# Kernel optimization log

Measured on AMD Instinct MI355X. Metric: run time of the kernel, lower is better.

The kernel has to match this reference:

```python
import jax, jax.numpy as jnp
import numpy as np

B, CIN, COUT, H, W, KK = 1, 32, 64, 181, 360, 4
NNZ_PER, NNZ_PER1 = 9, 4


def _make_psi(rng, K, H, W, nnz_per):
    # Sparse DISCO basis in COO form for longitude 0 (shift-invariant in lon).
    E = K * H * nnz_per
    seg = np.repeat(np.arange(K * H, dtype=np.int32), nnz_per)  # k*H + ho
    ho = seg % H
    dlat = rng.integers(-1, 2, size=E).astype(np.int32)
    hi = np.clip(ho + dlat, 0, H - 1).astype(np.int32)
    wi = (rng.integers(-1, 2, size=E).astype(np.int32)) % W
    vals = (rng.normal(size=E) * 0.2).astype(np.float32)
    return seg, hi, wi, vals


def setup_inputs() -> dict:
    rng = np.random.default_rng(0)
    key = jax.random.key(0)
    ks = jax.random.split(key, 5)
    x = jax.random.normal(ks[0], (B, CIN, H, W), dtype=jnp.float32)
    # spherical quadrature weights: sin(colatitude) * cell area
    theta = np.linspace(0.0, np.pi, H)
    qw = (np.sin(theta) * (np.pi / (H - 1)) * (2.0 * np.pi / W)).astype(np.float32)
    qw = np.maximum(qw, 1e-8).reshape(H, 1)
    seg, hi, wi, vals = _make_psi(rng, KK, H, W, NNZ_PER)
    seg1, hi1, wi1, vals1 = _make_psi(rng, 1, H, W, NNZ_PER1)
    w_depth = jax.random.normal(ks[1], (CIN, KK), dtype=jnp.float32) / np.sqrt(KK)
    w_point = jax.random.normal(ks[2], (COUT, CIN), dtype=jnp.float32) / np.sqrt(CIN)
    bias = jax.random.normal(ks[3], (COUT,), dtype=jnp.float32) * 0.02
    return {
        "x": x,
        "quad_w": jnp.asarray(qw),
        "vals": jnp.asarray(vals),
        "seg": jnp.asarray(seg),
        "hi": jnp.asarray(hi),
        "wi": jnp.asarray(wi),
        "w_depth": w_depth,
        "vals1": jnp.asarray(vals1),
        "seg1": jnp.asarray(seg1),
        "hi1": jnp.asarray(hi1),
        "wi1": jnp.asarray(wi1),
        "w_point": w_point,
        "bias": bias,
        "K": KK,
    }


def _disco_contract(x, vals, seg, hi, wi, K):
    # x: [B,C,H,W]; COO psi at lon 0; out[b,c,k,ho,wo] =
    #   sum_{e: seg[e]==k*H+ho} vals[e] * x[b,c,hi[e],(wi[e]+wo) mod W]
    Bq, C, Hq, Wq = x.shape
    rows = x[:, :, hi, :]                                        # [B,C,E,W]
    col = (wi[:, None] + jnp.arange(Wq, dtype=wi.dtype)[None, :]) % Wq  # [E,W]
    rolled = jnp.take_along_axis(rows, col[None, None, :, :], axis=3)   # [B,C,E,W]
    weighted = rolled * vals[None, None, :, None]
    out = jax.ops.segment_sum(weighted.transpose(2, 0, 1, 3), seg,
                              num_segments=K * Hq)               # [K*H,B,C,W]
    return out.reshape(K, Hq, Bq, C, Wq).transpose(2, 3, 0, 1, 4)  # [B,C,K,H,W]


def reference(x, quad_w, vals, seg, hi, wi, w_depth, vals1, seg1, hi1, wi1,
              w_point, bias, K):
    # depthwise DISCO conv (groups=C_in, no bias)
    xq = x * quad_w                                   # quadrature weighting
    xd = _disco_contract(xq, vals, seg, hi, wi, K)    # [B,C,K,H,W]
    y = jnp.einsum("ck,bckhw->bchw", w_depth, xd)     # per-channel K mix
    # pointwise DISCO conv (kernel_shape=1) = CLinear
    yq = y * quad_w
    z = _disco_contract(yq, vals1, seg1, hi1, wi1, 1)[:, :, 0]  # [B,C,H,W]
    out = jnp.einsum("oc,bchw->bohw", w_point, z) + bias[None, :, None, None]
    return out
```

## Files before the change

kernel.cpp:

```cpp
#include <hip/hip_runtime.h>


#define H_    181
#define W_    360
#define CIN_  32
#define COUT_ 64
#define K_    4
#define NNZ_  9
#define NNZ1_ 4
#define HW_   (H_*W_)
#define NT_   (NNZ1_*K_*NNZ_)

__global__ __launch_bounds__(256) void sepconv_one(
    const float* __restrict__ x, const float* __restrict__ quad_w,
    const float* __restrict__ vals, const int* __restrict__ hi,
    const int* __restrict__ wi, const float* __restrict__ w_depth,
    const float* __restrict__ vals1, const int* __restrict__ hi1,
    const int* __restrict__ wi1, const float* __restrict__ w_point,
    const float* __restrict__ bias, float* __restrict__ out)
{
    const int bx = blockIdx.x;
    const int h  = (bx & 7) * 23 + (bx >> 3);
    if (h >= H_) return;
    const int seg = blockIdx.y;
    const int w0  = seg * 64;
    const int pxn = (seg == 5) ? 40 : 64;
    const int gn  = pxn >> 2;
    const int tid = threadIdx.x;

    __shared__ float Tval[NT_];
    __shared__ int   Tbin[NT_];
    __shared__ float S[K_][25];
    __shared__ float C[CIN_][25];
    __shared__ float zs[64][33];

    if (tid < NT_) {
        const int a   = tid / 36;
        const int rem = tid - a * 36;
        const int k   = rem / 9;
        const int j   = rem - k * 9;
        const int e1  = h * NNZ1_ + a;
        const int m   = hi1[e1];
        const int w1  = wi1[e1];
        const int d1  = (w1 == 1) ? 1 : ((w1 == 0) ? 0 : -1);
        const int e   = (k * H_ + m) * NNZ_ + j;
        const int r   = hi[e];
        const int ww  = wi[e];
        const int d   = (ww == 1) ? 1 : ((ww == 0) ? 0 : -1);
        Tval[tid] = vals1[e1] * quad_w[m] * vals[e] * quad_w[r];
        Tbin[tid] = (r - h + 2) * 5 + (d1 + d + 2);
    }
    __syncthreads();

    if (tid < K_ * 25) {
        const int k   = tid / 25;
        const int bin = tid - k * 25;
        float s = 0.f;
        #pragma unroll
        for (int a = 0; a < NNZ1_; ++a)
            #pragma unroll
            for (int j = 0; j < NNZ_; ++j) {
                const int t2 = a * 36 + k * 9 + j;
                if (Tbin[t2] == bin) s += Tval[t2];
            }
        S[k][bin] = s;
    }
    __syncthreads();

    for (int i = tid; i < CIN_ * 25; i += 256) {
        const int c = i / 25, bin = i - c * 25;
        float acc = 0.f;
        #pragma unroll
        for (int k = 0; k < K_; ++k) acc += w_depth[c * K_ + k] * S[k][bin];
        C[c][bin] = acc;
    }
    __syncthreads();

    int rowoff[5];
    #pragma unroll
    for (int rb = 0; rb < 5; ++rb) {
        int r = h - 2 + rb;
        r = (r < 0) ? 0 : ((r > H_ - 1) ? H_ - 1 : r);
        rowoff[rb] = r * W_;
    }

    for (int q = tid; q < CIN_ * 16; q += 256) {
        const int c = q >> 4;
        const int g = q & 15;
        if (g < gn) {
            const int bw = w0 + g * 4;
            const int cA = (bw + W_ - 4) % W_;
            const int cB = bw;
            const int cC = (bw + 4) % W_;
            const float* xc = x + c * HW_;
            const float* Cc = &C[c][0];

            float a0 = 0.f, a1 = 0.f, a2 = 0.f, a3 = 0.f;
            #pragma unroll
            for (int rb = 0; rb < 5; ++rb) {
                const float* xr = xc + rowoff[rb];
                const float4 vA = *(const float4*)(xr + cA);
                const float4 vB = *(const float4*)(xr + cB);
                const float4 vC = *(const float4*)(xr + cC);
                const float k0 = Cc[rb * 5 + 0], k1 = Cc[rb * 5 + 1],
                            k2 = Cc[rb * 5 + 2], k3 = Cc[rb * 5 + 3],
                            k4 = Cc[rb * 5 + 4];
                a0 += k0 * vA.z + k1 * vA.w + k2 * vB.x + k3 * vB.y + k4 * vB.z;
                a1 += k0 * vA.w + k1 * vB.x + k2 * vB.y + k3 * vB.z + k4 * vB.w;
                a2 += k0 * vB.x + k1 * vB.y + k2 * vB.z + k3 * vB.w + k4 * vC.x;
                a3 += k0 * vB.y + k1 * vB.z + k2 * vB.w + k3 * vC.x + k4 * vC.y;
            }
            const int p = g * 4;
            zs[p + 0][c] = a0;
            zs[p + 1][c] = a1;
            zs[p + 2][c] = a2;
            zs[p + 3][c] = a3;
        }
    }
    __syncthreads();

    const int j  = tid & 63;
    const int oh = tid >> 6;
    if (j < pxn) {
        float zr[CIN_];
        #pragma unroll
        for (int c = 0; c < CIN_; ++c) zr[c] = zs[j][c];

        const float* wp = w_point + oh * 16 * CIN_;
        float* op = out + oh * 16 * HW_ + h * W_ + w0 + j;
        #pragma unroll 4
        for (int oo = 0; oo < 16; ++oo) {
            float acc = bias[oh * 16 + oo];
            #pragma unroll
            for (int c = 0; c < CIN_; ++c) acc += wp[oo * CIN_ + c] * zr[c];
            op[oo * HW_] = acc;
        }
    }
}

extern "C" void kernel_launch(void* const* d_in, const int* in_sizes, int n_in,
                              void* d_out, int out_size, void* d_ws, size_t ws_size,
                              hipStream_t stream) {
    const float* x       = (const float*)d_in[0];
    const float* quad_w  = (const float*)d_in[1];
    const float* vals    = (const float*)d_in[2];
    const int*   hi      = (const int*)d_in[4];
    const int*   wi      = (const int*)d_in[5];
    const float* w_depth = (const float*)d_in[6];
    const float* vals1   = (const float*)d_in[7];
    const int*   hi1     = (const int*)d_in[9];
    const int*   wi1     = (const int*)d_in[10];
    const float* w_point = (const float*)d_in[11];
    const float* bias    = (const float*)d_in[12];

    sepconv_one<<<dim3(184, 6), 256, 0, stream>>>(
        x, quad_w, vals, hi, wi, w_depth, vals1, hi1, wi1,
        w_point, bias, (float*)d_out);
}
```

Baseline: 118.8 us.

## Process two longitude segments per block, prefetching the second during the first GEMV

Each block now handles two 64-wide longitude segments instead of one, halving the grid. The per-row stencil-coefficient setup (Tval/S/C tables) is amortized over two segments, and the global loads for the second segment's stencil are issued before the first segment's pointwise GEMV so their latency overlaps that compute. The cost is higher register pressure from two 15-float4 prefetch buffers, which may reduce occupancy, and fewer blocks for the GPU to spread across CUs.

```diff
diff --git a/kernel.cpp b/kernel.cpp
--- a/kernel.cpp
+++ b/kernel.cpp
@@ -22,17 +22,14 @@
     const int bx = blockIdx.x;
     const int h  = (bx & 7) * 23 + (bx >> 3);
     if (h >= H_) return;
-    const int seg = blockIdx.y;
-    const int w0  = seg * 64;
-    const int pxn = (seg == 5) ? 40 : 64;
-    const int gn  = pxn >> 2;
+    const int sp  = blockIdx.y;
     const int tid = threadIdx.x;
 
     __shared__ float Tval[NT_];
     __shared__ int   Tbin[NT_];
     __shared__ float S[K_][25];
     __shared__ float C[CIN_][25];
-    __shared__ float zs[64][33];
+    __shared__ float zs[2][64][33];
 
     if (tid < NT_) {
         const int a   = tid / 36;
@@ -84,58 +81,107 @@
         rowoff[rb] = r * W_;
     }
 
-    for (int q = tid; q < CIN_ * 16; q += 256) {
-        const int c = q >> 4;
-        const int g = q & 15;
-        if (g < gn) {
-            const int bw = w0 + g * 4;
-            const int cA = (bw + W_ - 4) % W_;
-            const int cB = bw;
-            const int cC = (bw + 4) % W_;
-            const float* xc = x + c * HW_;
-            const float* Cc = &C[c][0];
-
-            float a0 = 0.f, a1 = 0.f, a2 = 0.f, a3 = 0.f;
-            #pragma unroll
-            for (int rb = 0; rb < 5; ++rb) {
-                const float* xr = xc + rowoff[rb];
-                const float4 vA = *(const float4*)(xr + cA);
-                const float4 vB = *(const float4*)(xr + cB);
-                const float4 vC = *(const float4*)(xr + cC);
-                const float k0 = Cc[rb * 5 + 0], k1 = Cc[rb * 5 + 1],
-                            k2 = Cc[rb * 5 + 2], k3 = Cc[rb * 5 + 3],
-                            k4 = Cc[rb * 5 + 4];
-                a0 += k0 * vA.z + k1 * vA.w + k2 * vB.x + k3 * vB.y + k4 * vB.z;
-                a1 += k0 * vA.w + k1 * vB.x + k2 * vB.y + k3 * vB.z + k4 * vB.w;
-                a2 += k0 * vB.x + k1 * vB.y + k2 * vB.z + k3 * vB.w + k4 * vC.x;
-                a3 += k0 * vB.y + k1 * vB.z + k2 * vB.w + k3 * vC.x + k4 * vC.y;
-            }
-            const int p = g * 4;
-            zs[p + 0][c] = a0;
-            zs[p + 1][c] = a1;
-            zs[p + 2][c] = a2;
-            zs[p + 3][c] = a3;
-        }
-    }
-    __syncthreads();
-
+    const int g  = tid & 15;
+    const int c0 = tid >> 4;
+    const int c1 = c0 + 16;
     const int j  = tid & 63;
     const int oh = tid >> 6;
-    if (j < pxn) {
-        float zr[CIN_];
-        #pragma unroll
-        for (int c = 0; c < CIN_; ++c) zr[c] = zs[j][c];
-
-        const float* wp = w_point + oh * 16 * CIN_;
-        float* op = out + oh * 16 * HW_ + h * W_ + w0 + j;
-        #pragma unroll 4
-        for (int oo = 0; oo < 16; ++oo) {
-            float acc = bias[oh * 16 + oo];
+
+    const int seg0 = sp * 2 + 0;
+    const int seg1 = sp * 2 + 1;
+    const int gn1  = (seg1 == 5) ? 10 : 16;
+
+    auto load_item = [&](int c, int bw, float4* Lv) {
+        const int cA = (bw + W_ - 4) % W_;
+        const int cB = bw;
+        const int cC = (bw + 4) % W_;
+        const float* xc = x + c * HW_;
+        #pragma unroll
+        for (int rb = 0; rb < 5; ++rb) {
+            const float* xr = xc + rowoff[rb];
+            Lv[rb * 3 + 0] = *(const float4*)(xr + cA);
+            Lv[rb * 3 + 1] = *(const float4*)(xr + cB);
+            Lv[rb * 3 + 2] = *(const float4*)(xr + cC);
+        }
+    };
+    auto fma_item = [&](int c, const float4* Lv, float* a) {
+        const float* Cc = &C[c][0];
+        a[0] = a[1] = a[2] = a[3] = 0.f;
+        #pragma unroll
+        for (int rb = 0; rb < 5; ++rb) {
+            const float4 vA = Lv[rb * 3 + 0];
+            const float4 vB = Lv[rb * 3 + 1];
+            const float4 vC = Lv[rb * 3 + 2];
+            const float k0 = Cc[rb * 5 + 0], k1 = Cc[rb * 5 + 1],
+                        k2 = Cc[rb * 5 + 2], k3 = Cc[rb * 5 + 3],
+                        k4 = Cc[rb * 5 + 4];
+            a[0] += k0 * vA.z + k1 * vA.w + k2 * vB.x + k3 * vB.y + k4 * vB.z;
+            a[1] += k0 * vA.w + k1 * vB.x + k2 * vB.y + k3 * vB.z + k4 * vB.w;
+            a[2] += k0 * vB.x + k1 * vB.y + k2 * vB.z + k3 * vB.w + k4 * vC.x;
+            a[3] += k0 * vB.y + k1 * vB.z + k2 * vB.w + k3 * vC.x + k4 * vC.y;
+        }
+    };
+    auto gemv = [&](int t, int seg) {
+        const int w0  = seg * 64;
+        const int pxn = (seg == 5) ? 40 : 64;
+        if (j < pxn) {
+            float zr[CIN_];
             #pragma unroll
-            for (int c = 0; c < CIN_; ++c) acc += wp[oo * CIN_ + c] * zr[c];
-            op[oo * HW_] = acc;
-        }
-    }
+            for (int c = 0; c < CIN_; ++c) zr[c] = zs[t][j][c];
+            const float* wp = w_point + oh * 16 * CIN_;
+            float* op = out + oh * 16 * HW_ + h * W_ + w0 + j;
+            #pragma unroll 4
+            for (int oo = 0; oo < 16; ++oo) {
+                float acc = bias[oh * 16 + oo];
+                #pragma unroll
+                for (int c = 0; c < CIN_; ++c)
+                    acc += wp[oo * CIN_ + c] * zr[c];
+                op[oo * HW_] = acc;
+            }
+        }
+    };
+
+    {
+        const int bw = seg0 * 64 + g * 4;
+        float4 L0[15], L1[15];
+        load_item(c0, bw, L0);
+        load_item(c1, bw, L1);
+        float a0[4], a1[4];
+        fma_item(c0, L0, a0);
+        fma_item(c1, L1, a1);
+        const int p = g * 4;
+        #pragma unroll
+        for (int u = 0; u < 4; ++u) {
+            zs[0][p + u][c0] = a0[u];
+            zs[0][p + u][c1] = a1[u];
+        }
+    }
+    __syncthreads();
+
+    float4 P0[15], P1[15];
+    const bool act1 = (g < gn1);
+    const int  bw1  = seg1 * 64 + g * 4;
+    if (act1) {
+        load_item(c0, bw1, P0);
+        load_item(c1, bw1, P1);
+    }
+
+    gemv(0, seg0);
+
+    if (act1) {
+        float a0[4], a1[4];
+        fma_item(c0, P0, a0);
+        fma_item(c1, P1, a1);
+        const int p = g * 4;
+        #pragma unroll
+        for (int u = 0; u < 4; ++u) {
+            zs[1][p + u][c0] = a0[u];
+            zs[1][p + u][c1] = a1[u];
+        }
+    }
+    __syncthreads();
+
+    gemv(1, seg1);
 }
 
 extern "C" void kernel_launch(void* const* d_in, const int* in_sizes, int n_in,
@@ -153,7 +199,7 @@
     const float* w_point = (const float*)d_in[11];
     const float* bias    = (const float*)d_in[12];
 
-    sepconv_one<<<dim3(184, 6), 256, 0, stream>>>(
+    sepconv_one<<<dim3(184, 3), 256, 0, stream>>>(
         x, quad_w, vals, hi, wi, w_depth, vals1, hi1, wi1,
         w_point, bias, (float*)d_out);
 }
```

Result: slower. 124.8 us (+5.1%).

## Prefetch input rows into registers before basis setup and double block size

Applied to the files above, without the earlier changes.

Each thread now issues its 15 float4 global loads of the input stencil at kernel entry, before the sparse-basis table construction and reductions. This overlaps the global-memory latency with the shared-memory setup phases. The block grows to 512 threads so each thread handles one (channel, group) pair and eight output channels instead of sixteen. The cost is 60 extra live registers per thread across the setup phase, which may lower occupancy under the larger launch bound.

```diff
diff --git a/kernel.cpp b/kernel.cpp
--- a/kernel.cpp
+++ b/kernel.cpp
@@ -11,7 +11,7 @@
 #define HW_   (H_*W_)
 #define NT_   (NNZ1_*K_*NNZ_)
 
-__global__ __launch_bounds__(256) void sepconv_one(
+__global__ __launch_bounds__(512) void sepconv_one(
     const float* __restrict__ x, const float* __restrict__ quad_w,
     const float* __restrict__ vals, const int* __restrict__ hi,
     const int* __restrict__ wi, const float* __restrict__ w_depth,
@@ -33,6 +33,35 @@
     __shared__ float S[K_][25];
     __shared__ float C[CIN_][25];
     __shared__ float zs[64][33];
+
+    const int g = tid & 15;
+    const int c = tid >> 4;
+    const bool act = (g < gn);
+
+    int rowoff[5];
+    #pragma unroll
+    for (int rb = 0; rb < 5; ++rb) {
+        int r = h - 2 + rb;
+        r = (r < 0) ? 0 : ((r > H_ - 1) ? H_ - 1 : r);
+        rowoff[rb] = r * W_;
+    }
+
+    const int bw = w0 + g * 4;
+    const int cA = (bw + W_ - 4) % W_;
+    const int cB = bw;
+    const int cC = (bw + 4) % W_;
+
+    float4 L[15];
+    if (act) {
+        const float* xc = x + c * HW_;
+        #pragma unroll
+        for (int rb = 0; rb < 5; ++rb) {
+            const float* xr = xc + rowoff[rb];
+            L[rb * 3 + 0] = *(const float4*)(xr + cA);
+            L[rb * 3 + 1] = *(const float4*)(xr + cB);
+            L[rb * 3 + 2] = *(const float4*)(xr + cC);
+        }
+    }
 
     if (tid < NT_) {
         const int a   = tid / 36;
@@ -67,55 +96,44 @@
     }
     __syncthreads();
 
-    for (int i = tid; i < CIN_ * 25; i += 256) {
-        const int c = i / 25, bin = i - c * 25;
+    if (tid < CIN_ * 25) {
+        const int cc = tid / 25, bin = tid - cc * 25;
         float acc = 0.f;
         #pragma unroll
-        for (int k = 0; k < K_; ++k) acc += w_depth[c * K_ + k] * S[k][bin];
-        C[c][bin] = acc;
+        for (int k = 0; k < K_; ++k) acc += w_depth[cc * K_ + k] * S[k][bin];
+        C[cc][bin] = acc;
+    }
+    if (tid + 512 < CIN_ * 25) {
+        const int i2 = tid + 512;
+        const int cc = i2 / 25, bin = i2 - cc * 25;
+        float acc = 0.f;
+        #pragma unroll
+        for (int k = 0; k < K_; ++k) acc += w_depth[cc * K_ + k] * S[k][bin];
+        C[cc][bin] = acc;
     }
     __syncthreads();
 
-    int rowoff[5];
-    #pragma unroll
-    for (int rb = 0; rb < 5; ++rb) {
-        int r = h - 2 + rb;
-        r = (r < 0) ? 0 : ((r > H_ - 1) ? H_ - 1 : r);
-        rowoff[rb] = r * W_;
-    }
-
-    for (int q = tid; q < CIN_ * 16; q += 256) {
-        const int c = q >> 4;
-        const int g = q & 15;
-        if (g < gn) {
-            const int bw = w0 + g * 4;
-            const int cA = (bw + W_ - 4) % W_;
-            const int cB = bw;
-            const int cC = (bw + 4) % W_;
-            const float* xc = x + c * HW_;
-            const float* Cc = &C[c][0];
-
-            float a0 = 0.f, a1 = 0.f, a2 = 0.f, a3 = 0.f;
-            #pragma unroll
-            for (int rb = 0; rb < 5; ++rb) {
-                const float* xr = xc + rowoff[rb];
-                const float4 vA = *(const float4*)(xr + cA);
-                const float4 vB = *(const float4*)(xr + cB);
-                const float4 vC = *(const float4*)(xr + cC);
-                const float k0 = Cc[rb * 5 + 0], k1 = Cc[rb * 5 + 1],
-                            k2 = Cc[rb * 5 + 2], k3 = Cc[rb * 5 + 3],
-                            k4 = Cc[rb * 5 + 4];
-                a0 += k0 * vA.z + k1 * vA.w + k2 * vB.x + k3 * vB.y + k4 * vB.z;
-                a1 += k0 * vA.w + k1 * vB.x + k2 * vB.y + k3 * vB.z + k4 * vB.w;
-                a2 += k0 * vB.x + k1 * vB.y + k2 * vB.z + k3 * vB.w + k4 * vC.x;
-                a3 += k0 * vB.y + k1 * vB.z + k2 * vB.w + k3 * vC.x + k4 * vC.y;
-            }
-            const int p = g * 4;
-            zs[p + 0][c] = a0;
-            zs[p + 1][c] = a1;
-            zs[p + 2][c] = a2;
-            zs[p + 3][c] = a3;
+    if (act) {
+        const float* Cc = &C[c][0];
+        float a0 = 0.f, a1 = 0.f, a2 = 0.f, a3 = 0.f;
+        #pragma unroll
+        for (int rb = 0; rb < 5; ++rb) {
+            const float4 vA = L[rb * 3 + 0];
+            const float4 vB = L[rb * 3 + 1];
+            const float4 vC = L[rb * 3 + 2];
+            const float k0 = Cc[rb * 5 + 0], k1 = Cc[rb * 5 + 1],
+                        k2 = Cc[rb * 5 + 2], k3 = Cc[rb * 5 + 3],
+                        k4 = Cc[rb * 5 + 4];
+            a0 += k0 * vA.z + k1 * vA.w + k2 * vB.x + k3 * vB.y + k4 * vB.z;
+            a1 += k0 * vA.w + k1 * vB.x + k2 * vB.y + k3 * vB.z + k4 * vB.w;
+            a2 += k0 * vB.x + k1 * vB.y + k2 * vB.z + k3 * vB.w + k4 * vC.x;
+            a3 += k0 * vB.y + k1 * vB.z + k2 * vB.w + k3 * vC.x + k4 * vC.y;
         }
+        const int p = g * 4;
+        zs[p + 0][c] = a0;
+        zs[p + 1][c] = a1;
+        zs[p + 2][c] = a2;
+        zs[p + 3][c] = a3;
     }
     __syncthreads();
 
@@ -124,15 +142,16 @@
     if (j < pxn) {
         float zr[CIN_];
         #pragma unroll
-        for (int c = 0; c < CIN_; ++c) zr[c] = zs[j][c];
+        for (int cc = 0; cc < CIN_; ++cc) zr[cc] = zs[j][cc];
 
-        const float* wp = w_point + oh * 16 * CIN_;
-        float* op = out + oh * 16 * HW_ + h * W_ + w0 + j;
-        #pragma unroll 4
-        for (int oo = 0; oo < 16; ++oo) {
-            float acc = bias[oh * 16 + oo];
+        const float* wp = w_point + oh * 8 * CIN_;
+        float* op = out + oh * 8 * HW_ + h * W_ + w0 + j;
+        #pragma unroll
+        for (int oo = 0; oo < 8; ++oo) {
+            float acc = bias[oh * 8 + oo];
             #pragma unroll
-            for (int c = 0; c < CIN_; ++c) acc += wp[oo * CIN_ + c] * zr[c];
+            for (int cc = 0; cc < CIN_; ++cc)
+                acc += wp[oo * CIN_ + cc] * zr[cc];
             op[oo * HW_] = acc;
         }
     }
@@ -153,7 +172,7 @@
     const float* w_point = (const float*)d_in[11];
     const float* bias    = (const float*)d_in[12];
 
-    sepconv_one<<<dim3(184, 6), 256, 0, stream>>>(
+    sepconv_one<<<dim3(184, 6), 512, 0, stream>>>(
         x, quad_w, vals, hi, wi, w_depth, vals1, hi1, wi1,
         w_point, bias, (float*)d_out);
 }
```

Measured after the change: 116.1 us (median of 2 runs). -2.2%, faster.
